# Performance work log

Measured on AMD Instinct MI355X. Metric: run time of the kernel, lower is better.

## Reference

```python
import jax, jax.numpy as jnp
import numpy as np

B, T, D, H = 2, 2048, 1024, 8
HD = D // H

def setup_inputs() -> dict:
    key = jax.random.key(0)
    ks = jax.random.split(key, 6)
    s = 1.0 / np.sqrt(D)
    x = jax.random.normal(ks[0], (B, T, D), dtype=jnp.float32)
    Wq = jax.random.normal(ks[1], (D, D), dtype=jnp.float32) * s
    Wk = jax.random.normal(ks[2], (D, D), dtype=jnp.float32) * s
    Wv = jax.random.normal(ks[3], (D, D), dtype=jnp.float32) * s
    Wo = jax.random.normal(ks[4], (D, D), dtype=jnp.float32) * s
    bo = jnp.zeros((D,), dtype=jnp.float32)
    # theta[i] = 1 / 10000**(2i/H) as in _init_parameters
    theta = (1.0 / (10000.0 ** (2.0 * jnp.arange(H, dtype=jnp.float32) / H))).astype(jnp.float32)
    gamma = jnp.ones((D,), dtype=jnp.float32)   # group_norm weight
    beta = jnp.zeros((D,), dtype=jnp.float32)   # group_norm bias
    return {"x": x, "Wq": Wq, "Wk": Wk, "Wv": Wv, "Wo": Wo, "bo": bo,
            "theta": theta, "gamma": gamma, "beta": beta}

def reference(x, Wq, Wk, Wv, Wo, bo, theta, gamma, beta):
    b, t, d = x.shape
    h = theta.shape[0]
    hd = d // h
    q = (x @ Wq).reshape(b, t, h, hd)
    k = (x @ Wk).reshape(b, t, h, hd)
    v = (x @ Wv).reshape(b, t, h, hd)

    # decay mask: vectorized closed form of the O(T^2) python loop.
    # mask[i,j] = mean_h exp(-theta_h * (i-j)) for j<=i else 0
    pos = jnp.arange(t, dtype=jnp.float32)
    n = pos[:, None] - pos[None, :]                       # (T,T) i-j
    nn = jnp.maximum(n, 0.0)
    decay_mask = jnp.where(n >= 0,
                           jnp.mean(jnp.exp(-theta[None, None, :] * nn[:, :, None]), axis=-1),
                           0.0)                            # (T,T)

    scores = jnp.einsum('bthd,bshd->bths', q, k) / np.sqrt(hd)   # (B,T,H,T)
    scores = scores * decay_mask[None, :, None, :]
    causal = (n >= 0)[None, :, None, :]
    scores = jnp.where(causal, scores, -jnp.inf)
    retention = jax.nn.softmax(scores, axis=-1)
    out = jnp.einsum('bths,bshd->bthd', retention, v)            # (B,T,H,HD)

    # GroupNorm(num_heads, d_model): normalize each head's hd-chunk per token
    mu = out.mean(axis=-1, keepdims=True)
    var = out.var(axis=-1, keepdims=True)
    out = (out - mu) / jnp.sqrt(var + 1e-5)
    out = out.reshape(b, t, d) * gamma + beta

    return out @ Wo + bo
```

## Files before the change

### kernel.cpp

```cpp
#include <hip/hip_runtime.h>

#define B_SZ  2
#define T_SEQ 2048
#define D_MOD 1024
#define NH    8
#define HD    128

typedef __attribute__((ext_vector_type(8))) short short8;
typedef __attribute__((ext_vector_type(4))) float f32x4;

__device__ __forceinline__ short f2bf(float f) {
  unsigned u = __float_as_uint(f);
  unsigned r = u + 0x7fffu + ((u >> 16) & 1u);
  return (short)(r >> 16);
}

__device__ __forceinline__ void gld_lds16(const short* g, short* l) {
  __builtin_amdgcn_global_load_lds(
      (const __attribute__((address_space(1))) void*)g,
      (__attribute__((address_space(3))) void*)l, 16, 0, 0);
}

__global__ void decay_kernel(const float* __restrict__ theta,
                             float* __restrict__ dm) {
  int n = blockIdx.x * 256 + threadIdx.x;
  if (n >= T_SEQ) return;
  float nf = (float)n;
  float s = 0.f;
#pragma unroll
  for (int h = 0; h < NH; h++) s += __expf(-theta[h] * nf);
  dm[n] = s * (0.08838834764831845f / 8.0f);
}

__global__ __launch_bounds__(256) void cvt_x(const float* __restrict__ x,
                                             short* __restrict__ xb) {
  int i = (blockIdx.x * 256 + threadIdx.x) * 8;
  float4 a = *(const float4*)(x + i);
  float4 b = *(const float4*)(x + i + 4);
  short8 o;
  o[0] = f2bf(a.x); o[1] = f2bf(a.y); o[2] = f2bf(a.z); o[3] = f2bf(a.w);
  o[4] = f2bf(b.x); o[5] = f2bf(b.y); o[6] = f2bf(b.z); o[7] = f2bf(b.w);
  *(short8*)(xb + i) = o;
}

__global__ __launch_bounds__(256) void cvt_w(const float* __restrict__ Wq,
                                             const float* __restrict__ Wk,
                                             const float* __restrict__ Wv,
                                             const float* __restrict__ Wo,
                                             short* __restrict__ wt) {
  __shared__ float t[32][33];
  const int z = blockIdx.z;
  const float* __restrict__ W = (z == 0) ? Wq : (z == 1) ? Wk : (z == 2) ? Wv : Wo;
  short* __restrict__ dst = wt + (size_t)z * D_MOD * D_MOD;
  const int k0 = blockIdx.x * 32, n0 = blockIdx.y * 32;
  const int tx = threadIdx.x & 31, ty = threadIdx.x >> 5;
#pragma unroll
  for (int i = 0; i < 4; i++)
    t[ty * 4 + i][tx] = W[(size_t)(k0 + ty * 4 + i) * D_MOD + n0 + tx];
  __syncthreads();
#pragma unroll
  for (int i = 0; i < 4; i++)
    dst[(size_t)(n0 + ty * 4 + i) * D_MOD + k0 + tx] = f2bf(t[tx][ty * 4 + i]);
}

__global__ __launch_bounds__(256, 3) void gemm_qkv(
    const short* __restrict__ xb, const short* __restrict__ wt,
    short* __restrict__ qb, short* __restrict__ kb, short* __restrict__ vb) {
  __shared__ __align__(16) short As[128 * 32];
  __shared__ __align__(16) short Bs[128 * 32];
  const int tid = threadIdx.x;
  const int l = tid & 63, w = tid >> 6;
  const int wr = w >> 1, wc = w & 1;
  const int row0 = blockIdx.x * 128;
  const int h = blockIdx.y;
  const int col0 = h * 128;
  const short* __restrict__ Wt = wt + (size_t)blockIdx.z * D_MOD * D_MOD;
  short* __restrict__ dst = (blockIdx.z == 0) ? qb : (blockIdx.z == 1) ? kb : vb;

  f32x4 acc[4][4];
#pragma unroll
  for (int m = 0; m < 4; m++)
#pragma unroll
    for (int n = 0; n < 4; n++) acc[m][n] = (f32x4){0.f, 0.f, 0.f, 0.f};

  const int cA = w * 2;
  const int sr = l >> 2;
  const int skq = (l & 3) << 3;

#pragma unroll
  for (int i = 0; i < 2; i++) {
    int c = cA + i;
    gld_lds16(xb + (size_t)(row0 + c * 16 + sr) * D_MOD + skq, As + c * 512);
    gld_lds16(Wt + (size_t)(col0 + c * 16 + sr) * D_MOD + skq, Bs + c * 512);
  }
  for (int ks = 0; ks < 32; ks++) {
    __syncthreads();
    short8 af[4], bf[4];
#pragma unroll
    for (int m = 0; m < 4; m++)
      af[m] = *(const short8*)&As[(wr * 64 + m * 16 + (l & 15)) * 32 + (l >> 4) * 8];
#pragma unroll
    for (int n = 0; n < 4; n++)
      bf[n] = *(const short8*)&Bs[(wc * 64 + n * 16 + (l & 15)) * 32 + (l >> 4) * 8];
#pragma unroll
    for (int m = 0; m < 4; m++)
#pragma unroll
      for (int n = 0; n < 4; n++)
        acc[m][n] =
            __builtin_amdgcn_mfma_f32_16x16x32_bf16(af[m], bf[n], acc[m][n], 0, 0, 0);
    __syncthreads();
    if (ks < 31) {
      const int k0 = (ks + 1) * 32;
#pragma unroll
      for (int i = 0; i < 2; i++) {
        int c = cA + i;
        gld_lds16(xb + (size_t)(row0 + c * 16 + sr) * D_MOD + k0 + skq, As + c * 512);
        gld_lds16(Wt + (size_t)(col0 + c * 16 + sr) * D_MOD + k0 + skq, Bs + c * 512);
      }
    }
  }
#pragma unroll
  for (int m = 0; m < 4; m++) {
#pragma unroll
    for (int j = 0; j < 4; j++) {
      int row = row0 + wr * 64 + m * 16 + (l >> 4) * 4 + j;
      int bb = row >> 11, t = row & (T_SEQ - 1);
      size_t base = ((size_t)(bb * NH + h) * T_SEQ + t) * HD + wc * 64 + (l & 15);
#pragma unroll
      for (int n = 0; n < 4; n++) dst[base + n * 16] = f2bf(acc[m][n][j]);
    }
  }
}

__global__ __launch_bounds__(256, 3) void gemm_out(
    const short* __restrict__ yb, const short* __restrict__ wot,
    const float* __restrict__ bias, float* __restrict__ out) {
  __shared__ __align__(16) short As[128 * 32];
  __shared__ __align__(16) short Bs[128 * 32];
  const int tid = threadIdx.x;
  const int l = tid & 63, w = tid >> 6;
  const int wr = w >> 1, wc = w & 1;
  const int row0 = blockIdx.x * 128;
  const int col0 = blockIdx.y * 128;

  f32x4 acc[4][4];
#pragma unroll
  for (int m = 0; m < 4; m++)
#pragma unroll
    for (int n = 0; n < 4; n++) acc[m][n] = (f32x4){0.f, 0.f, 0.f, 0.f};

  const int cA = w * 2;
  const int sr = l >> 2;
  const int skq = (l & 3) << 3;

#pragma unroll
  for (int i = 0; i < 2; i++) {
    int c = cA + i;
    gld_lds16(yb + (size_t)(row0 + c * 16 + sr) * D_MOD + skq, As + c * 512);
    gld_lds16(wot + (size_t)(col0 + c * 16 + sr) * D_MOD + skq, Bs + c * 512);
  }
  for (int ks = 0; ks < 32; ks++) {
    __syncthreads();
    short8 af[4], bf[4];
#pragma unroll
    for (int m = 0; m < 4; m++)
      af[m] = *(const short8*)&As[(wr * 64 + m * 16 + (l & 15)) * 32 + (l >> 4) * 8];
#pragma unroll
    for (int n = 0; n < 4; n++)
      bf[n] = *(const short8*)&Bs[(wc * 64 + n * 16 + (l & 15)) * 32 + (l >> 4) * 8];
#pragma unroll
    for (int m = 0; m < 4; m++)
#pragma unroll
      for (int n = 0; n < 4; n++)
        acc[m][n] =
            __builtin_amdgcn_mfma_f32_16x16x32_bf16(af[m], bf[n], acc[m][n], 0, 0, 0);
    __syncthreads();
    if (ks < 31) {
      const int k0 = (ks + 1) * 32;
#pragma unroll
      for (int i = 0; i < 2; i++) {
        int c = cA + i;
        gld_lds16(yb + (size_t)(row0 + c * 16 + sr) * D_MOD + k0 + skq, As + c * 512);
        gld_lds16(wot + (size_t)(col0 + c * 16 + sr) * D_MOD + k0 + skq, Bs + c * 512);
      }
    }
  }
#pragma unroll
  for (int m = 0; m < 4; m++) {
#pragma unroll
    for (int j = 0; j < 4; j++) {
      int row = row0 + wr * 64 + m * 16 + (l >> 4) * 4 + j;
#pragma unroll
      for (int n = 0; n < 4; n++) {
        int col = col0 + wc * 64 + n * 16 + (l & 15);
        out[(size_t)row * D_MOD + col] = acc[m][n][j] + bias[col];
      }
    }
  }
}

__global__ __launch_bounds__(256, 2) void attn_kernel(
    const short* __restrict__ qg, const short* __restrict__ kg,
    const short* __restrict__ vg, const float* __restrict__ dm_g,
    const float* __restrict__ gamma, const float* __restrict__ beta,
    short* __restrict__ yb) {
  __shared__ __align__(16) short KT[4 * 4 * 64 * 8];
  __shared__ __align__(16) short VT[8 * 2 * 64 * 8];
  __shared__ __align__(16) float P2[4][1024];
  __shared__ float dm_s[T_SEQ];

  const int tid = threadIdx.x;
  const int l = tid & 63, w = tid >> 6;
  const int lm = l & 15, lq = l >> 4;

  int qt = blockIdx.x & 31;
  const int h = (blockIdx.x >> 5) & 7;
  const int b = blockIdx.x >> 8;
  if (b) qt = 31 - qt;

  for (int i = tid; i < T_SEQ; i += 256) dm_s[i] = dm_g[i];

  const size_t hoff = (size_t)(b * NH + h) * T_SEQ * HD;
  const short* __restrict__ Qh = qg + hoff;
  const short* __restrict__ Kh = kg + hoff;
  const short* __restrict__ Vh = vg + hoff;

  short8 qf[4];
  {
    int row = qt * 64 + w * 16 + lm;
#pragma unroll
    for (int kc = 0; kc < 4; kc++)
      qf[kc] = *(const short8*)(Qh + (size_t)row * HD + kc * 32 + lq * 8);
  }

  f32x4 zero4 = {0.f, 0.f, 0.f, 0.f};
  f32x4 o[8];
#pragma unroll
  for (int cb = 0; cb < 8; cb++) o[cb] = zero4;
  float m_r[4], l_r[4];
#pragma unroll
  for (int r = 0; r < 4; r++) { m_r[r] = -1e30f; l_r[r] = 0.f; }

  const int i_row0 = qt * 64 + w * 16 + lq * 4;
  const int njt = qt + 1;

  __syncthreads();

  for (int jt = 0; jt < njt; jt++) {
    const int j0 = jt * 64;
#pragma unroll
    for (int kc = 0; kc < 4; kc++) {
      int jrow = j0 + w * 16 + lm;
      short8 kv = *(const short8*)(Kh + (size_t)jrow * HD + kc * 32 + lq * 8);
      *(short8*)&KT[((w * 4 + kc) * 64 + l) * 8] = kv;
    }
    {
      const int d0 = (tid & 63) * 2;
#pragma unroll
      for (int pass = 0; pass < 2; pass++) {
        const int jl = (w + pass * 4) * 8;
        unsigned vals[8];
#pragma unroll
        for (int jj = 0; jj < 8; jj++)
          vals[jj] = *(const unsigned*)(Vh + (size_t)(j0 + jl + jj) * HD + d0);
        const int kc2 = jl >> 5;
        const int bq = (jl >> 3) & 3;
#pragma unroll
        for (int dd = 0; dd < 2; dd++) {
          const int d = d0 + dd;
          short8 col;
#pragma unroll
          for (int jj = 0; jj < 8; jj++)
            col[jj] = (short)(dd ? (vals[jj] >> 16) : (vals[jj] & 0xffffu));
          *(short8*)&VT[(((d >> 4) * 2 + kc2) * 64 + bq * 16 + (d & 15)) * 8] =
              col;
        }
      }
    }
    __syncthreads();

    float s[4][4];
#pragma unroll
    for (int jb = 0; jb < 4; jb++) {
      f32x4 acc = zero4;
#pragma unroll
      for (int kc = 0; kc < 4; kc++) {
        short8 kf = *(const short8*)&KT[((jb * 4 + kc) * 64 + l) * 8];
        acc = __builtin_amdgcn_mfma_f32_16x16x32_bf16(qf[kc], kf, acc, 0, 0, 0);
      }
      const int j = j0 + jb * 16 + lm;
#pragma unroll
      for (int r = 0; r < 4; r++) {
        int delta = (i_row0 + r) - j;
        s[jb][r] = (delta >= 0) ? acc[r] * dm_s[delta] : -__builtin_inff();
      }
    }

    float fac[4];
#pragma unroll
    for (int r = 0; r < 4; r++) {
      float mx = fmaxf(fmaxf(s[0][r], s[1][r]), fmaxf(s[2][r], s[3][r]));
      mx = fmaxf(mx, __shfl_xor(mx, 1));
      mx = fmaxf(mx, __shfl_xor(mx, 2));
      mx = fmaxf(mx, __shfl_xor(mx, 4));
      mx = fmaxf(mx, __shfl_xor(mx, 8));
      float mnew = fmaxf(m_r[r], mx);
      fac[r] = __expf(m_r[r] - mnew);
      m_r[r] = mnew;
    }
    float lsum[4] = {0.f, 0.f, 0.f, 0.f};
#pragma unroll
    for (int jb = 0; jb < 4; jb++) {
      const int jl2 = jb * 16 + lm;
      const int pbase = (jl2 >> 5) * 512 + ((jl2 & 31) >> 3) * 128 + (jl2 & 7);
#pragma unroll
      for (int r = 0; r < 4; r++) {
        float pv = __expf(s[jb][r] - m_r[r]);
        lsum[r] += pv;
        P2[w][pbase + (lq * 4 + r) * 8] = pv;
      }
    }
#pragma unroll
    for (int r = 0; r < 4; r++) {
      float sm = lsum[r];
      sm += __shfl_xor(sm, 1); sm += __shfl_xor(sm, 2);
      sm += __shfl_xor(sm, 4); sm += __shfl_xor(sm, 8);
      l_r[r] = l_r[r] * fac[r] + sm;
    }
#pragma unroll
    for (int cb = 0; cb < 8; cb++)
#pragma unroll
      for (int r = 0; r < 4; r++) o[cb][r] *= fac[r];

#pragma unroll
    for (int kc2 = 0; kc2 < 2; kc2++) {
      f32x4 pa0 = *(const f32x4*)&P2[w][kc2 * 512 + l * 8];
      f32x4 pa1 = *(const f32x4*)&P2[w][kc2 * 512 + l * 8 + 4];
      short8 pb;
#pragma unroll
      for (int e = 0; e < 4; e++) {
        pb[e] = f2bf(pa0[e]);
        pb[e + 4] = f2bf(pa1[e]);
      }
#pragma unroll
      for (int cb = 0; cb < 8; cb++) {
        short8 vf = *(const short8*)&VT[((cb * 2 + kc2) * 64 + l) * 8];
        o[cb] = __builtin_amdgcn_mfma_f32_16x16x32_bf16(pb, vf, o[cb], 0, 0, 0);
      }
    }
    __syncthreads();
  }

  float mu[4], rstd[4];
#pragma unroll
  for (int r = 0; r < 4; r++) {
    float inv = 1.0f / l_r[r];
    float sum = 0.f, sq = 0.f;
#pragma unroll
    for (int cb = 0; cb < 8; cb++) {
      float v2 = o[cb][r] * inv;
      o[cb][r] = v2;
      sum += v2;
      sq += v2 * v2;
    }
    sum += __shfl_xor(sum, 1); sum += __shfl_xor(sum, 2);
    sum += __shfl_xor(sum, 4); sum += __shfl_xor(sum, 8);
    sq += __shfl_xor(sq, 1); sq += __shfl_xor(sq, 2);
    sq += __shfl_xor(sq, 4); sq += __shfl_xor(sq, 8);
    float m2 = sum * (1.f / 128.f);
    mu[r] = m2;
    rstd[r] = rsqrtf(sq * (1.f / 128.f) - m2 * m2 + 1e-5f);
  }
  const int trow = qt * 64 + w * 16 + lq * 4;
#pragma unroll
  for (int cb = 0; cb < 8; cb++) {
    const int dcol = h * HD + cb * 16 + lm;
    const float g = gamma[dcol], be = beta[dcol];
#pragma unroll
    for (int r = 0; r < 4; r++) {
      float val = (o[cb][r] - mu[r]) * rstd[r] * g + be;
      yb[(size_t)(b * T_SEQ + trow + r) * D_MOD + dcol] = f2bf(val);
    }
  }
}

extern "C" void kernel_launch(void* const* d_in, const int* in_sizes, int n_in,
                              void* d_out, int out_size, void* d_ws,
                              size_t ws_size, hipStream_t stream) {
  const float* x     = (const float*)d_in[0];
  const float* Wq    = (const float*)d_in[1];
  const float* Wk    = (const float*)d_in[2];
  const float* Wv    = (const float*)d_in[3];
  const float* Wo    = (const float*)d_in[4];
  const float* bo    = (const float*)d_in[5];
  const float* theta = (const float*)d_in[6];
  const float* gamma = (const float*)d_in[7];
  const float* beta  = (const float*)d_in[8];
  float* out = (float*)d_out;

  char* ws = (char*)d_ws;
  const size_t MB = 1024 * 1024;
  short* qb = (short*)(ws + 0 * MB);
  short* kb = (short*)(ws + 8 * MB);
  short* vb = (short*)(ws + 16 * MB);
  short* yb = (short*)(ws + 24 * MB);
  short* xb = (short*)(ws + 32 * MB);
  short* wt = (short*)(ws + 40 * MB);
  float* dm = (float*)(ws + 48 * MB);

  decay_kernel<<<dim3(8), dim3(256), 0, stream>>>(theta, dm);
  cvt_x<<<dim3(2048), dim3(256), 0, stream>>>(x, xb);
  cvt_w<<<dim3(32, 32, 4), dim3(256), 0, stream>>>(Wq, Wk, Wv, Wo, wt);
  gemm_qkv<<<dim3(32, 8, 3), dim3(256), 0, stream>>>(xb, wt, qb, kb, vb);
  attn_kernel<<<dim3(512), dim3(256), 0, stream>>>(qb, kb, vb, dm, gamma, beta, yb);
  gemm_out<<<dim3(32, 8), dim3(256), 0, stream>>>(
      yb, wt + (size_t)3 * D_MOD * D_MOD, bo, out);
}
```

Before: 248.9 us.

## Double-buffer K/V tiles in attention with async LDS loads and prefetch

Attention now uses double-buffered K and V shared tiles. The next K tile is prefetched straight into LDS with global_load_lds, and the next V tile is read into registers before compute, then transposed into the other buffer afterwards, so one barrier per iteration is removed and loads overlap the MFMA work. The decay mask is read from global/L1 instead of being staged in shared memory. s_setprio is raised around the MFMA sections. In exchange, LDS use and register pressure go up (16 V registers held across compute), and the decay lookups become uncached-in-LDS global loads inside the inner loop.

```diff
diff --git a/kernel.cpp b/kernel.cpp
--- a/kernel.cpp
+++ b/kernel.cpp
@@ -204,10 +204,9 @@
     const short* __restrict__ vg, const float* __restrict__ dm_g,
     const float* __restrict__ gamma, const float* __restrict__ beta,
     short* __restrict__ yb) {
-  __shared__ __align__(16) short KT[4 * 4 * 64 * 8];
-  __shared__ __align__(16) short VT[8 * 2 * 64 * 8];
+  __shared__ __align__(16) short KT[2][8192];
+  __shared__ __align__(16) short VT[2][8192];
   __shared__ __align__(16) float P2[4][1024];
-  __shared__ float dm_s[T_SEQ];
 
   const int tid = threadIdx.x;
   const int l = tid & 63, w = tid >> 6;
@@ -218,8 +217,6 @@
   const int b = blockIdx.x >> 8;
   if (b) qt = 31 - qt;
 
-  for (int i = tid; i < T_SEQ; i += 256) dm_s[i] = dm_g[i];
-
   const size_t hoff = (size_t)(b * NH + h) * T_SEQ * HD;
   const short* __restrict__ Qh = qg + hoff;
   const short* __restrict__ Kh = kg + hoff;
@@ -243,58 +240,77 @@
 
   const int i_row0 = qt * 64 + w * 16 + lq * 4;
   const int njt = qt + 1;
-
+  const int d0 = l * 2;
+
+  unsigned vv[16];
+
+#pragma unroll
+  for (int kc = 0; kc < 4; kc++)
+    gld_lds16(Kh + (size_t)(w * 16 + lm) * HD + kc * 32 + lq * 8,
+              &KT[0][(w * 4 + kc) * 512]);
+#pragma unroll
+  for (int p = 0; p < 2; p++)
+#pragma unroll
+    for (int jj = 0; jj < 8; jj++)
+      vv[p * 8 + jj] =
+          *(const unsigned*)(Vh + (size_t)((w + p * 4) * 8 + jj) * HD + d0);
+#pragma unroll
+  for (int p = 0; p < 2; p++) {
+    const int jl = (w + p * 4) * 8;
+    const int kc2 = jl >> 5, bq = (jl >> 3) & 3;
+#pragma unroll
+    for (int dd = 0; dd < 2; dd++) {
+      const int d = d0 + dd;
+      short8 col;
+#pragma unroll
+      for (int jj = 0; jj < 8; jj++) {
+        unsigned u = vv[p * 8 + jj];
+        col[jj] = (short)(dd ? (u >> 16) : (u & 0xffffu));
+      }
+      *(short8*)&VT[0][(((d >> 4) * 2 + kc2) * 64 + bq * 16 + (d & 15)) * 8] = col;
+    }
+  }
   __syncthreads();
 
+  int cur = 0;
   for (int jt = 0; jt < njt; jt++) {
     const int j0 = jt * 64;
-#pragma unroll
-    for (int kc = 0; kc < 4; kc++) {
-      int jrow = j0 + w * 16 + lm;
-      short8 kv = *(const short8*)(Kh + (size_t)jrow * HD + kc * 32 + lq * 8);
-      *(short8*)&KT[((w * 4 + kc) * 64 + l) * 8] = kv;
-    }
-    {
-      const int d0 = (tid & 63) * 2;
-#pragma unroll
-      for (int pass = 0; pass < 2; pass++) {
-        const int jl = (w + pass * 4) * 8;
-        unsigned vals[8];
+    const int nxt = cur ^ 1;
+    const bool pf = (jt + 1) < njt;
+
+    if (pf) {
+      const int jn = j0 + 64;
+#pragma unroll
+      for (int kc = 0; kc < 4; kc++)
+        gld_lds16(Kh + (size_t)(jn + w * 16 + lm) * HD + kc * 32 + lq * 8,
+                  &KT[nxt][(w * 4 + kc) * 512]);
+#pragma unroll
+      for (int p = 0; p < 2; p++)
 #pragma unroll
         for (int jj = 0; jj < 8; jj++)
-          vals[jj] = *(const unsigned*)(Vh + (size_t)(j0 + jl + jj) * HD + d0);
-        const int kc2 = jl >> 5;
-        const int bq = (jl >> 3) & 3;
-#pragma unroll
-        for (int dd = 0; dd < 2; dd++) {
-          const int d = d0 + dd;
-          short8 col;
-#pragma unroll
-          for (int jj = 0; jj < 8; jj++)
-            col[jj] = (short)(dd ? (vals[jj] >> 16) : (vals[jj] & 0xffffu));
-          *(short8*)&VT[(((d >> 4) * 2 + kc2) * 64 + bq * 16 + (d & 15)) * 8] =
-              col;
-        }
-      }
-    }
-    __syncthreads();
+          vv[p * 8 + jj] =
+              *(const unsigned*)(Vh + (size_t)(jn + (w + p * 4) * 8 + jj) * HD + d0);
+    }
 
     float s[4][4];
+    __builtin_amdgcn_s_setprio(1);
 #pragma unroll
     for (int jb = 0; jb < 4; jb++) {
       f32x4 acc = zero4;
 #pragma unroll
       for (int kc = 0; kc < 4; kc++) {
-        short8 kf = *(const short8*)&KT[((jb * 4 + kc) * 64 + l) * 8];
+        short8 kf = *(const short8*)&KT[cur][((jb * 4 + kc) * 64 + l) * 8];
         acc = __builtin_amdgcn_mfma_f32_16x16x32_bf16(qf[kc], kf, acc, 0, 0, 0);
       }
       const int j = j0 + jb * 16 + lm;
 #pragma unroll
       for (int r = 0; r < 4; r++) {
         int delta = (i_row0 + r) - j;
-        s[jb][r] = (delta >= 0) ? acc[r] * dm_s[delta] : -__builtin_inff();
-      }
-    }
+        float dmv = dm_g[delta < 0 ? 0 : delta];
+        s[jb][r] = (delta >= 0) ? acc[r] * dmv : -__builtin_inff();
+      }
+    }
+    __builtin_amdgcn_s_setprio(0);
 
     float fac[4];
 #pragma unroll
@@ -332,6 +348,7 @@
 #pragma unroll
       for (int r = 0; r < 4; r++) o[cb][r] *= fac[r];
 
+    __builtin_amdgcn_s_setprio(1);
 #pragma unroll
     for (int kc2 = 0; kc2 < 2; kc2++) {
       f32x4 pa0 = *(const f32x4*)&P2[w][kc2 * 512 + l * 8];
@@ -344,11 +361,33 @@
       }
 #pragma unroll
       for (int cb = 0; cb < 8; cb++) {
-        short8 vf = *(const short8*)&VT[((cb * 2 + kc2) * 64 + l) * 8];
+        short8 vf = *(const short8*)&VT[cur][((cb * 2 + kc2) * 64 + l) * 8];
         o[cb] = __builtin_amdgcn_mfma_f32_16x16x32_bf16(pb, vf, o[cb], 0, 0, 0);
       }
     }
+    __builtin_amdgcn_s_setprio(0);
+
+    if (pf) {
+#pragma unroll
+      for (int p = 0; p < 2; p++) {
+        const int jl = (w + p * 4) * 8;
+        const int kc2 = jl >> 5, bq = (jl >> 3) & 3;
+#pragma unroll
+        for (int dd = 0; dd < 2; dd++) {
+          const int d = d0 + dd;
+          short8 col;
+#pragma unroll
+          for (int jj = 0; jj < 8; jj++) {
+            unsigned u = vv[p * 8 + jj];
+            col[jj] = (short)(dd ? (u >> 16) : (u & 0xffffu));
+          }
+          *(short8*)&VT[nxt][(((d >> 4) * 2 + kc2) * 64 + bq * 16 + (d & 15)) * 8] =
+              col;
+        }
+      }
+    }
     __syncthreads();
+    cur = nxt;
   }
 
   float mu[4], rstd[4];
```

Result: slower. 267.3 us (+7.4%).
